# Kernel optimization log

Hardware: AMD Instinct MI355X
Metric: run time of the kernel (lower is better)

The kernel has to match this reference:

```python
import jax, jax.numpy as jnp
import numpy as np

D = 4096       # embed_dim
H = 16         # num_heads
HD = D // H    # head_dim = 256
MLP_H = int(D * 2.0)  # 8192
L_V = 2048
L_T = 1024
GAMMA = 0.6
NOISE_STD = 0.07
TEMP = 0.05
LN_EPS = 1e-5


def setup_inputs() -> dict:
    key = jax.random.key(0)
    ks = jax.random.split(key, 16)
    s = 0.02
    return {
        "vision_feature": jax.random.normal(ks[0], (L_V, D), jnp.float32),
        "text_embed": jax.random.normal(ks[1], (L_T, D), jnp.float32),
        "attention_mask": jnp.zeros((L_T,), jnp.float32),  # additive mask, 0 = attend
        "noise": jax.random.normal(ks[2], (L_V,), jnp.float32),
        "Wq": jax.random.normal(ks[3], (D, D), jnp.float32) * s,
        "bq": jnp.zeros((D,), jnp.float32),
        "Wk": jax.random.normal(ks[4], (D, D), jnp.float32) * s,
        "bk": jnp.zeros((D,), jnp.float32),
        "Wv": jax.random.normal(ks[5], (D, D), jnp.float32) * s,
        "bv": jnp.zeros((D,), jnp.float32),
        "Wo": jax.random.normal(ks[6], (D, D), jnp.float32) * s,
        "bo": jnp.zeros((D,), jnp.float32),
        "ln_w": jnp.ones((D,), jnp.float32),
        "ln_b": jnp.zeros((D,), jnp.float32),
        "W1": jax.random.normal(ks[7], (MLP_H, D), jnp.float32) * s,
        "b1": jnp.zeros((MLP_H,), jnp.float32),
        "W2": jax.random.normal(ks[8], (1, MLP_H), jnp.float32) * s,
        "b2": jnp.zeros((1,), jnp.float32),
    }


def reference(vision_feature, text_embed, attention_mask, noise,
              Wq, bq, Wk, bk, Wv, bv, Wo, bo, ln_w, ln_b, W1, b1, W2, b2):
    # --- cross attention (vision queries over text keys/values) ---
    q = (vision_feature @ Wq.T + bq).reshape(L_V, H, HD)
    k = (text_embed @ Wk.T + bk).reshape(L_T, H, HD)
    v = (text_embed @ Wv.T + bv).reshape(L_T, H, HD)
    logits = jnp.einsum('qhd,khd->hqk', q, k) / np.float32(np.sqrt(HD))
    logits = logits + attention_mask[None, None, :]  # additive attn_mask
    attn = jax.nn.softmax(logits, axis=-1)
    ctx = jnp.einsum('hqk,khd->qhd', attn, v).reshape(L_V, D)
    attn_out = ctx @ Wo.T + bo
    # --- residual + layernorm ---
    x = vision_feature + attn_out
    mu = jnp.mean(x, axis=-1, keepdims=True)
    var = jnp.mean(jnp.square(x - mu), axis=-1, keepdims=True)
    xn = (x - mu) / jnp.sqrt(var + LN_EPS) * ln_w + ln_b
    # --- tiny MLP scorer ---
    h = jax.nn.gelu(xn @ W1.T + b1, approximate=False)
    weight_scores = (h @ W2.T + b2)[:, 0] + noise * NOISE_STD
    # --- temperature softmax over all tokens, top-p (gamma) selection ---
    p = jax.nn.softmax(weight_scores / TEMP, axis=0)
    order = jnp.argsort(-p)           # descending sort indices
    cum = jnp.cumsum(p[order])
    keep = cum <= GAMMA               # threshold_index prefix mask
    gathered = vision_feature[order]  # [L_V, D]
    # fixed-shape stand-in for indices[:threshold_index] gather:
    # valid selected rows are the nonzero prefix
    return jnp.where(keep[:, None], gathered, jnp.zeros((), gathered.dtype))
```

## Files before the change

kernel.cpp:

```cpp
#include <hip/hip_runtime.h>
#include <math.h>


#define LV   2048
#define LT   1024
#define DIM  4096
#define NHD  16
#define HDD  256
#define MLPH 8192

typedef __attribute__((ext_vector_type(8))) short bfx8;
typedef __attribute__((ext_vector_type(4))) float fx4;
typedef unsigned short u16;

__device__ __forceinline__ float wave_sum(float v){
#pragma unroll
  for (int o = 32; o > 0; o >>= 1) v += __shfl_xor(v, o);
  return v;
}
__device__ __forceinline__ float wave_max(float v){
#pragma unroll
  for (int o = 32; o > 0; o >>= 1) v = fmaxf(v, __shfl_xor(v, o));
  return v;
}

__device__ __forceinline__ void splitpack(const float4 a, const float4 b,
                                          bfx8* hi, bfx8* lo){
  float f[8] = {a.x,a.y,a.z,a.w, b.x,b.y,b.z,b.w};
  union { bfx8 v; unsigned u[4]; } H, L;
#pragma unroll
  for (int p = 0; p < 4; ++p){
    unsigned u0 = __float_as_uint(f[2*p]);
    unsigned u1 = __float_as_uint(f[2*p+1]);
    H.u[p] = (u0 >> 16) | (u1 & 0xffff0000u);
    float h0 = __uint_as_float(u0 & 0xffff0000u);
    float h1 = __uint_as_float(u1 & 0xffff0000u);
    unsigned v0 = __float_as_uint(f[2*p]   - h0);
    unsigned v1 = __float_as_uint(f[2*p+1] - h1);
    L.u[p] = (v0 >> 16) | (v1 & 0xffff0000u);
  }
  *hi = H.v; *lo = L.v;
}

__device__ __forceinline__ void glds16(const void* g, void* l){
  __builtin_amdgcn_global_load_lds(
      (const __attribute__((address_space(1))) unsigned int*)g,
      (__attribute__((address_space(3))) unsigned int*)l, 16, 0, 0);
}

__global__ __launch_bounds__(256)
void repack_kernel(const float* __restrict__ src, u16* __restrict__ hi,
                   u16* __restrict__ lo, int Kc, int ktsh)
{
  const long long e = ((long long)blockIdx.x * 256 + threadIdx.x) * 8;
  const int T = (int)(e >> 9);
  const int L = (int)(e >> 3) & 63;
  const int rt = T >> ktsh, kt = T & ((1 << ktsh) - 1);
  const int r = (rt << 4) + (L & 15);
  const int k = (kt << 5) + ((L >> 4) << 3);
  const float* p = src + (long long)r * Kc + k;
  bfx8 h, l;
  splitpack(*(const float4*)p, *(const float4*)(p + 4), &h, &l);
  *(bfx8*)(hi + e) = h;
  *(bfx8*)(lo + e) = l;
}

template<int GELU, int TRANSC>
__global__ __launch_bounds__(256)
void mgemm(const u16* __restrict__ Ah, const u16* __restrict__ Al, int aKT, long long aZe,
           const u16* __restrict__ Bh, const u16* __restrict__ Bl, int bKT, long long bZe,
           float* __restrict__ C, int ldc, long long cZe,
           const float* __restrict__ bias,
           int nx, int KT, int kt0, int zkt, float alpha)
{
  __shared__ bfx8 lbuf[32][64];
  const int tid  = threadIdx.x;
  const int lane = tid & 63;
  const int wv   = tid >> 6;
  const int wr   = wv >> 1, wc = wv & 1;
  const int nwg  = gridDim.x;
  const int id   = blockIdx.x;
  int bm, bn;
  {
    const int my = nwg / nx;
    if (((nx & 3) == 0) && ((my & 1) == 0) && ((nwg & 7) == 0)){
      const int rm = my >> 1, rn = nx >> 2;
      const int x  = id & 7;
      const int j  = id >> 3;
      bm = ((x >> 2) * rm) + j / rn;
      bn = ((x & 3) * rn) + j % rn;
    } else if (((my & 7) == 0) && ((nwg & 7) == 0)){
      const int rm = my >> 3;
      const int x = id & 7, j = id >> 3;
      bm = x * rm + j / nx;
      bn = j % nx;
    } else { bm = id / nx; bn = id % nx; }
  }
  const int m0 = bm << 7;
  const int n0 = bn << 7;
  const int z    = blockIdx.z;
  const u16* Ahz = Ah + (long long)z * aZe;
  const u16* Alz = Al + (long long)z * aZe;
  const u16* Bhz = Bh + (long long)z * bZe;
  const u16* Blz = Bl + (long long)z * bZe;
  C += (long long)z * cZe;
  const int ktb  = kt0 + z * zkt;
  const int rtA0 = m0 >> 4, rtB0 = n0 >> 4;

  const fx4 zz = {0.f, 0.f, 0.f, 0.f};
  fx4 acc[4][4];
#pragma unroll
  for (int i = 0; i < 4; ++i)
#pragma unroll
    for (int j = 0; j < 4; ++j) acc[i][j] = zz;

  const u16* wbase = (wv == 0) ? Ahz : (wv == 1) ? Alz : (wv == 2) ? Bhz : Blz;
  const int  wrt0  = (wv < 2) ? rtA0 : rtB0;
  const int  wKT   = (wv < 2) ? aKT  : bKT;

  for (int t = 0; t < KT; ++t){
#pragma unroll
    for (int q = 0; q < 8; ++q){
      const u16* g = wbase + ((long long)(wrt0 + q) * wKT + (ktb + t)) * 512
                     + lane * 8;
      glds16((const void*)g, (void*)&lbuf[wv * 8 + q][0]);
    }
    __syncthreads();
    bfx8 ah[4], al[4], bh[4], bl[4];
#pragma unroll
    for (int i = 0; i < 4; ++i){
      ah[i] = lbuf[     wr*4 + i][lane];
      al[i] = lbuf[ 8 + wr*4 + i][lane];
      bh[i] = lbuf[16 + wc*4 + i][lane];
      bl[i] = lbuf[24 + wc*4 + i][lane];
    }
#pragma unroll
    for (int i = 0; i < 4; ++i)
#pragma unroll
      for (int j = 0; j < 4; ++j){
        acc[i][j] = __builtin_amdgcn_mfma_f32_16x16x32_bf16(ah[i], bl[j], acc[i][j], 0, 0, 0);
        acc[i][j] = __builtin_amdgcn_mfma_f32_16x16x32_bf16(al[i], bh[j], acc[i][j], 0, 0, 0);
        acc[i][j] = __builtin_amdgcn_mfma_f32_16x16x32_bf16(ah[i], bh[j], acc[i][j], 0, 0, 0);
      }
    __syncthreads();
  }

#pragma unroll
  for (int i = 0; i < 4; ++i){
    const int row0 = m0 + wr*64 + i*16 + ((lane >> 4) << 2);
#pragma unroll
    for (int j = 0; j < 4; ++j){
      const int col = n0 + wc*64 + j*16 + (lane & 15);
      const float bb = bias ? bias[col] : 0.0f;
      if (TRANSC){
        float4 o;
        o.x = alpha*acc[i][j][0] + bb;
        o.y = alpha*acc[i][j][1] + bb;
        o.z = alpha*acc[i][j][2] + bb;
        o.w = alpha*acc[i][j][3] + bb;
        *(float4*)(C + (size_t)col*ldc + row0) = o;
      } else {
#pragma unroll
        for (int r = 0; r < 4; ++r){
          float v = alpha*acc[i][j][r] + bb;
          if (GELU) v = 0.5f*v*(1.0f + erff(v*0.70710678f));
          C[(size_t)(row0 + r)*ldc + col] = v;
        }
      }
    }
  }
}

template<int GELU, int TRANSC>
__global__ __launch_bounds__(256)
void mgemm_fb(const float* __restrict__ A, long long aZ, int lda,
              const float* __restrict__ B, long long bZ, int ldb,
              float* __restrict__ C, long long cZ, int ldc,
              const float* __restrict__ bias, int Kd, float alpha)
{
  __shared__ bfx8 AhS[512], AlS[512], BhS[512], BlS[512];
  const int tid  = threadIdx.x;
  const int lane = tid & 63;
  const int wv   = tid >> 6;
  const int wr   = wv >> 1, wc = wv & 1;
  const int m0 = blockIdx.y * 128, n0 = blockIdx.x * 128;
  A += (long long)blockIdx.z * aZ;
  B += (long long)blockIdx.z * bZ;
  C += (long long)blockIdx.z * cZ;

  const fx4 zz = {0.f, 0.f, 0.f, 0.f};
  fx4 acc[4][4];
#pragma unroll
  for (int i = 0; i < 4; ++i)
#pragma unroll
    for (int j = 0; j < 4; ++j) acc[i][j] = zz;

  for (int k0 = 0; k0 < Kd; k0 += 32){
    __syncthreads();
#pragma unroll
    for (int pass = 0; pass < 2; ++pass){
      const int s = pass*256 + tid;
      const int m = ((s >> 6) << 4) + (s & 15);
      const int j = (s >> 4) & 3;
      const float* pA = A + (size_t)(m0 + m)*lda + k0 + j*8;
      splitpack(*(const float4*)pA, *(const float4*)(pA + 4), &AhS[s], &AlS[s]);
      const float* pB = B + (size_t)(n0 + m)*ldb + k0 + j*8;
      splitpack(*(const float4*)pB, *(const float4*)(pB + 4), &BhS[s], &BlS[s]);
    }
    __syncthreads();
    bfx8 ah[4], al[4], bh[4], bl[4];
#pragma unroll
    for (int i = 0; i < 4; ++i){
      ah[i] = AhS[(wr*4 + i)*64 + lane];
      al[i] = AlS[(wr*4 + i)*64 + lane];
      bh[i] = BhS[(wc*4 + i)*64 + lane];
      bl[i] = BlS[(wc*4 + i)*64 + lane];
    }
#pragma unroll
    for (int i = 0; i < 4; ++i)
#pragma unroll
      for (int j = 0; j < 4; ++j){
        acc[i][j] = __builtin_amdgcn_mfma_f32_16x16x32_bf16(ah[i], bl[j], acc[i][j], 0, 0, 0);
        acc[i][j] = __builtin_amdgcn_mfma_f32_16x16x32_bf16(al[i], bh[j], acc[i][j], 0, 0, 0);
        acc[i][j] = __builtin_amdgcn_mfma_f32_16x16x32_bf16(ah[i], bh[j], acc[i][j], 0, 0, 0);
      }
  }
#pragma unroll
  for (int i = 0; i < 4; ++i){
    const int row0 = m0 + wr*64 + i*16 + ((lane >> 4) << 2);
#pragma unroll
    for (int j = 0; j < 4; ++j){
      const int col = n0 + wc*64 + j*16 + (lane & 15);
      const float bb = bias ? bias[col] : 0.0f;
      if (TRANSC){
        float4 o;
        o.x = alpha*acc[i][j][0] + bb;
        o.y = alpha*acc[i][j][1] + bb;
        o.z = alpha*acc[i][j][2] + bb;
        o.w = alpha*acc[i][j][3] + bb;
        *(float4*)(C + (size_t)col*ldc + row0) = o;
      } else {
#pragma unroll
        for (int r = 0; r < 4; ++r){
          float v = alpha*acc[i][j][r] + bb;
          if (GELU) v = 0.5f*v*(1.0f + erff(v*0.70710678f));
          C[(size_t)(row0 + r)*ldc + col] = v;
        }
      }
    }
  }
}

__global__ __launch_bounds__(128)
void softmax_pack(const float* __restrict__ Lf, u16* __restrict__ ph,
                  u16* __restrict__ pl)
{
  __shared__ float rr[4];
  const int tid = threadIdx.x;
  const int h = blockIdx.x >> 11;
  const int m = blockIdx.x & 2047;
  const float* row = Lf + ((long long)h * 2048 + m) * 1024;
  const int k = tid * 8;
  float4 a = *(const float4*)(row + k);
  float4 b = *(const float4*)(row + k + 4);
  float v[8] = {a.x,a.y,a.z,a.w, b.x,b.y,b.z,b.w};
  float mx = v[0];
#pragma unroll
  for (int i = 1; i < 8; ++i) mx = fmaxf(mx, v[i]);
  mx = wave_max(mx);
  if ((tid & 63) == 0) rr[tid >> 6] = mx;
  __syncthreads();
  const float M = fmaxf(rr[0], rr[1]);
  float e[8], s = 0.0f;
#pragma unroll
  for (int i = 0; i < 8; ++i){ e[i] = expf(v[i] - M); s += e[i]; }
  s = wave_sum(s);
  if ((tid & 63) == 0) rr[2 + (tid >> 6)] = s;
  __syncthreads();
  const float S = rr[2] + rr[3];
  float4 p0 = make_float4(e[0]/S, e[1]/S, e[2]/S, e[3]/S);
  float4 p1 = make_float4(e[4]/S, e[5]/S, e[6]/S, e[7]/S);
  bfx8 hh, ll;
  splitpack(p0, p1, &hh, &ll);
  const int tile = (m >> 4) * 32 + (k >> 5);
  const int Lw = ((k >> 3) & 3) * 16 + (m & 15);
  const long long eoff = (long long)h * (2048ll*1024) + (long long)tile * 512 + Lw * 8;
  *(bfx8*)(ph + eoff) = hh;
  *(bfx8*)(pl + eoff) = ll;
}

__global__ __launch_bounds__(256)
void softmax_fb(float* __restrict__ X)
{
  __shared__ float r[8];
  const int tid = threadIdx.x;
  float* row = X + (size_t)blockIdx.x * 1024;
  float4 v = ((const float4*)row)[tid];
  float m = fmaxf(fmaxf(v.x,v.y), fmaxf(v.z,v.w));
  m = wave_max(m);
  if ((tid & 63) == 0) r[tid >> 6] = m;
  __syncthreads();
  m = fmaxf(fmaxf(r[0],r[1]), fmaxf(r[2],r[3]));
  float e0 = expf(v.x - m), e1 = expf(v.y - m), e2 = expf(v.z - m), e3 = expf(v.w - m);
  float s = (e0 + e1) + (e2 + e3);
  s = wave_sum(s);
  if ((tid & 63) == 0) r[4 + (tid >> 6)] = s;
  __syncthreads();
  s = (r[4] + r[5]) + (r[6] + r[7]);
  ((float4*)row)[tid] = make_float4(e0/s, e1/s, e2/s, e3/s);
}

template<int PACK>
__global__ __launch_bounds__(256)
void ln_kernel(const float* __restrict__ vis, const float* ao, float* xnf,
               u16* __restrict__ xh, u16* __restrict__ xl,
               const float* __restrict__ w, const float* __restrict__ b)
{
  __shared__ float r[8];
  __shared__ float stat[2];
  const int tid = threadIdx.x;
  const int m = blockIdx.x;
  const size_t base = (size_t)m * DIM + tid * 16;
  float x[16];
#pragma unroll
  for (int q = 0; q < 4; ++q){
    float4 a = *(const float4*)(vis + base + q*4);
    float4 c = *(const float4*)(ao  + base + q*4);
    x[q*4+0]=a.x+c.x; x[q*4+1]=a.y+c.y; x[q*4+2]=a.z+c.z; x[q*4+3]=a.w+c.w;
  }
  float s = 0.0f;
#pragma unroll
  for (int i = 0; i < 16; ++i) s += x[i];
  s = wave_sum(s);
  if ((tid & 63) == 0) r[tid >> 6] = s;
  __syncthreads();
  if (tid == 0) stat[0] = (r[0]+r[1]+r[2]+r[3]) * (1.0f/4096.0f);
  __syncthreads();
  const float mu = stat[0];
  float vs = 0.0f;
#pragma unroll
  for (int i = 0; i < 16; ++i){ float d = x[i]-mu; vs += d*d; }
  vs = wave_sum(vs);
  if ((tid & 63) == 0) r[4 + (tid >> 6)] = vs;
  __syncthreads();
  if (tid == 0) stat[1] = (r[4]+r[5]+r[6]+r[7]) * (1.0f/4096.0f);
  __syncthreads();
  const float inv = 1.0f / sqrtf(stat[1] + 1e-5f);
  const int col = tid * 16;
  float o[16];
#pragma unroll
  for (int q = 0; q < 4; ++q){
    float4 wv = *(const float4*)(w + col + q*4);
    float4 bv = *(const float4*)(b + col + q*4);
    o[q*4+0] = (x[q*4+0]-mu)*inv*wv.x + bv.x;
    o[q*4+1] = (x[q*4+1]-mu)*inv*wv.y + bv.y;
    o[q*4+2] = (x[q*4+2]-mu)*inv*wv.z + bv.z;
    o[q*4+3] = (x[q*4+3]-mu)*inv*wv.w + bv.w;
  }
  if (PACK){
#pragma unroll
    for (int q = 0; q < 2; ++q){
      const int k = col + q*8;
      float4 p0 = make_float4(o[q*8+0], o[q*8+1], o[q*8+2], o[q*8+3]);
      float4 p1 = make_float4(o[q*8+4], o[q*8+5], o[q*8+6], o[q*8+7]);
      bfx8 hh, ll;
      splitpack(p0, p1, &hh, &ll);
      const int tile = (m >> 4) * 128 + (k >> 5);
      const int Lw = ((k >> 3) & 3) * 16 + (m & 15);
      const long long e = (long long)tile * 512 + Lw * 8;
      *(bfx8*)(xh + e) = hh;
      *(bfx8*)(xl + e) = ll;
    }
  } else {
#pragma unroll
    for (int q = 0; q < 4; ++q)
      *(float4*)(xnf + base + q*4) = make_float4(o[q*4+0],o[q*4+1],o[q*4+2],o[q*4+3]);
  }
}

__global__ __launch_bounds__(256)
void score_kernel(const float* __restrict__ H1, const float* __restrict__ W2v,
                  const float* __restrict__ b2, const float* __restrict__ noise,
                  float* __restrict__ sc)
{
  __shared__ float r[4];
  const int tid = threadIdx.x;
  const float* h = H1 + (size_t)blockIdx.x * MLPH + tid * 32;
  const float* w = W2v + tid * 32;
  float s = 0.0f;
#pragma unroll
  for (int q = 0; q < 8; ++q){
    float4 a = *(const float4*)(h + q*4);
    float4 c = *(const float4*)(w + q*4);
    s += a.x*c.x + a.y*c.y + a.z*c.z + a.w*c.w;
  }
  s = wave_sum(s);
  if ((tid & 63) == 0) r[tid >> 6] = s;
  __syncthreads();
  if (tid == 0) sc[blockIdx.x] = (r[0]+r[1]+r[2]+r[3]) + b2[0] + noise[blockIdx.x]*0.07f;
}

__global__ __launch_bounds__(1024)
void select_kernel(const float* __restrict__ scores,
                   int* __restrict__ ord, int* __restrict__ kcount)
{
  __shared__ float sv[LV];
  __shared__ int   si[LV];
  __shared__ float red[32];
  __shared__ float stat[2];
  const int tid = threadIdx.x;
  for (int i = tid; i < LV; i += 1024){ sv[i] = scores[i] / 0.05f; si[i] = i; }
  __syncthreads();
  float m = -3.4e38f;
  for (int i = tid; i < LV; i += 1024) m = fmaxf(m, sv[i]);
  m = wave_max(m);
  if ((tid & 63) == 0) red[tid >> 6] = m;
  __syncthreads();
  if (tid == 0){
    float M = red[0];
    for (int w = 1; w < 16; ++w) M = fmaxf(M, red[w]);
    stat[0] = M;
  }
  __syncthreads();
  const float ymax = stat[0];
  float d = 0.0f;
  for (int i = tid; i < LV; i += 1024) d += expf(sv[i] - ymax);
  d = wave_sum(d);
  if ((tid & 63) == 0) red[16 + (tid >> 6)] = d;
  __syncthreads();
  if (tid == 0){
    float D = 0.0f;
    for (int w = 0; w < 16; ++w) D += red[16 + w];
    stat[1] = D;
  }
  __syncthreads();
  const float denom = stat[1];
  for (int size = 2; size <= LV; size <<= 1){
    for (int stride = size >> 1; stride > 0; stride >>= 1){
      __syncthreads();
      const int i = 2*tid - (tid & (stride - 1));
      const int j = i + stride;
      const bool up = ((i & size) == 0);
      float a = sv[i], b = sv[j];
      if ((a < b) == up){
        sv[i] = b; sv[j] = a;
        int ti = si[i]; si[i] = si[j]; si[j] = ti;
      }
    }
  }
  __syncthreads();
  for (int i = tid; i < LV; i += 1024) sv[i] = expf(sv[i] - ymax) / denom;
  __syncthreads();
  if (tid == 0){
    float c = 0.0f; int kc = LV;
    for (int j = 0; j < LV; ++j){
      c += sv[j];
      if (!((double)c <= 0.6)){ kc = j; break; }
    }
    *kcount = kc;
  }
  __syncthreads();
  for (int i = tid; i < LV; i += 1024) ord[i] = si[i];
}

__global__ __launch_bounds__(256)
void writer_kernel(const float* __restrict__ vis, const int* __restrict__ ord,
                   const int* __restrict__ kc, float* __restrict__ out)
{
  const int j = blockIdx.x;
  float4* dst = (float4*)(out + (size_t)j * DIM);
  if (j < kc[0]){
    const float4* src = (const float4*)(vis + (size_t)ord[j] * DIM);
    for (int i = threadIdx.x; i < DIM/4; i += 256) dst[i] = src[i];
  } else {
    const float4 z4 = make_float4(0.f,0.f,0.f,0.f);
    for (int i = threadIdx.x; i < DIM/4; i += 256) dst[i] = z4;
  }
}

extern "C" void kernel_launch(void* const* d_in, const int* in_sizes, int n_in,
                              void* d_out, int out_size, void* d_ws, size_t ws_size,
                              hipStream_t stream)
{
  (void)in_sizes; (void)n_in; (void)out_size;
  const float* vis  = (const float*)d_in[0];
  const float* txt  = (const float*)d_in[1];
  const float* mask = (const float*)d_in[2];
  const float* noise= (const float*)d_in[3];
  const float* Wq = (const float*)d_in[4];  const float* bq = (const float*)d_in[5];
  const float* Wk = (const float*)d_in[6];  const float* bk = (const float*)d_in[7];
  const float* Wv = (const float*)d_in[8];  const float* bv = (const float*)d_in[9];
  const float* Wo = (const float*)d_in[10]; const float* bo = (const float*)d_in[11];
  const float* lw = (const float*)d_in[12]; const float* lb = (const float*)d_in[13];
  const float* W1 = (const float*)d_in[14]; const float* b1 = (const float*)d_in[15];
  const float* W2 = (const float*)d_in[16]; const float* b2 = (const float*)d_in[17];
  float* out = (float*)d_out;
  const dim3 blk(256);
  const size_t MiB = 1u << 20;

  int Hc = 0;
  for (int h = 16; h >= 1; h >>= 1){
    size_t need = (192 + 16 * (size_t)h) * MiB;
    if (need <= ws_size){ Hc = h; break; }
  }

  if (Hc > 0){
    char* B0 = (char*)d_ws;
    u16* WSh  = (u16*)(B0 + 0);          u16* WSl  = (u16*)(B0 + 32*MiB);
    float* TMPf = (float*)(B0 + 64*MiB);
    u16* QCh  = (u16*)(B0 + 96*MiB);     u16* QCl  = (u16*)(B0 + 112*MiB);
    u16* VCh  = (u16*)(B0 + 128*MiB);    u16* VCl  = (u16*)(B0 + 144*MiB);
    u16* TCh  = (u16*)(B0 + 160*MiB);    u16* TCl  = (u16*)(B0 + 168*MiB);
    float* KF  = (float*)(B0 + 176*MiB);
    float* VTF = (float*)(B0 + 192*MiB);
    u16* VTCh = (u16*)(B0 + 176*MiB);    u16* VTCl = (u16*)(B0 + 184*MiB);
    float* Lf  = (float*)(B0 + 192*MiB);
    u16* PCh  = (u16*)(B0 + (192 + (size_t)Hc*8)*MiB);
    u16* PCl  = (u16*)(B0 + (192 + (size_t)Hc*12)*MiB);
    float* H1f = (float*)(B0 + 128*MiB);
    u16* XNh  = (u16*)(B0 + 96*MiB);     u16* XNl  = (u16*)(B0 + 112*MiB);
    float* SCf = (float*)(B0 + 192*MiB);
    int* ORD = (int*)(SCf + LV);
    int* KCp = ORD + LV;

    repack_kernel<<<dim3(4096), blk, 0, stream>>>(vis, VCh, VCl, 4096, 7);
    repack_kernel<<<dim3(2048), blk, 0, stream>>>(txt, TCh, TCl, 4096, 7);
    repack_kernel<<<dim3(8192), blk, 0, stream>>>(Wq, WSh, WSl, 4096, 7);
    mgemm<0,0><<<dim3(512,1,1), blk, 0, stream>>>(VCh, VCl, 128, 0, WSh, WSl, 128, 0,
        TMPf, 4096, 0, bq, 32, 128, 0, 0, 1.0f);
    repack_kernel<<<dim3(8192), blk, 0, stream>>>(Wk, WSh, WSl, 4096, 7);
    mgemm<0,0><<<dim3(256,1,1), blk, 0, stream>>>(TCh, TCl, 128, 0, WSh, WSl, 128, 0,
        KF, 4096, 0, bk, 32, 128, 0, 0, 1.0f);
    repack_kernel<<<dim3(8192), blk, 0, stream>>>(Wv, WSh, WSl, 4096, 7);
    mgemm<0,1><<<dim3(256,1,1), blk, 0, stream>>>(TCh, TCl, 128, 0, WSh, WSl, 128, 0,
        VTF, 1024, 0, bv, 32, 128, 0, 0, 1.0f);
    repack_kernel<<<dim3(4096), blk, 0, stream>>>(TMPf, QCh, QCl, 4096, 7);
    repack_kernel<<<dim3(2048), blk, 0, stream>>>(KF, TCh, TCl, 4096, 7);
    repack_kernel<<<dim3(2048), blk, 0, stream>>>(VTF, VTCh, VTCl, 1024, 5);
    const int NG = NHD / Hc;
    for (int g = 0; g < NG; ++g){
      mgemm<0,0><<<dim3(128,1,Hc), blk, 0, stream>>>(QCh, QCl, 128, 0, TCh, TCl, 128, 0,
          Lf, 1024, 2097152ll, mask, 8, 8, g*Hc*8, 8, 0.0625f);
      softmax_pack<<<dim3(Hc*2048), dim3(128), 0, stream>>>(Lf, PCh, PCl);
      mgemm<0,0><<<dim3(32,1,Hc), blk, 0, stream>>>(PCh, PCl, 32, 2097152ll,
          VTCh + (long long)g*Hc*262144, VTCl + (long long)g*Hc*262144, 32, 262144ll,
          TMPf + (long long)g*Hc*256, 4096, 256, nullptr, 2, 32, 0, 0, 1.0f);
    }
    repack_kernel<<<dim3(4096), blk, 0, stream>>>(TMPf, VCh, VCl, 4096, 7);
    repack_kernel<<<dim3(8192), blk, 0, stream>>>(Wo, WSh, WSl, 4096, 7);
    mgemm<0,0><<<dim3(512,1,1), blk, 0, stream>>>(VCh, VCl, 128, 0, WSh, WSl, 128, 0,
        TMPf, 4096, 0, bo, 32, 128, 0, 0, 1.0f);
    ln_kernel<1><<<dim3(LV), blk, 0, stream>>>(vis, TMPf, nullptr, XNh, XNl, lw, lb);
    repack_kernel<<<dim3(8192), blk, 0, stream>>>(W1, WSh, WSl, 4096, 7);
    mgemm<1,0><<<dim3(512,1,1), blk, 0, stream>>>(XNh, XNl, 128, 0, WSh, WSl, 128, 0,
        H1f, 8192, 0, b1, 32, 128, 0, 0, 1.0f);
    repack_kernel<<<dim3(8192), blk, 0, stream>>>(W1 + 16777216ll, WSh, WSl, 4096, 7);
    mgemm<1,0><<<dim3(512,1,1), blk, 0, stream>>>(XNh, XNl, 128, 0, WSh, WSl, 128, 0,
        H1f + 4096, 8192, 0, b1 + 4096, 32, 128, 0, 0, 1.0f);
    score_kernel<<<dim3(LV), blk, 0, stream>>>(H1f, W2, b2, noise, SCf);
    select_kernel<<<dim3(1), dim3(1024), 0, stream>>>(SCf, ORD, KCp);
    writer_kernel<<<dim3(LV), blk, 0, stream>>>(vis, ORD, KCp, out);
    return;
  }

  float* ws = (float*)d_ws;
  const long long OQ  = 0;
  const long long OK_ = (long long)LV * DIM;
  const long long OV  = OK_ + (long long)LT * DIM;
  const long long OC  = OV  + (long long)LT * DIM;
  const long long OL  = OC  + (long long)LV * DIM;
  const long long LSTRIDE = (long long)LV * LT;
  int Hf = 16;
  while (Hf > 1){
    size_t need = (size_t)(OL + (long long)Hf * LSTRIDE + 8192) * 4;
    if (need <= ws_size) break;
    Hf >>= 1;
  }
  float* Qw  = ws + OQ;
  float* Kw  = ws + OK_;
  float* Vt  = ws + OV;
  float* Cw  = ws + OC;
  float* Lw  = ws + OL;
  float* H1w = ws + OK_;
  float* SCw = ws + OL + (long long)Hf * LSTRIDE;
  int*   ORDw = (int*)(SCw + LV);
  int*   KCw  = ORDw + LV;

  mgemm_fb<0,0><<<dim3(DIM/128, LV/128, 1), blk, 0, stream>>>(vis,0,DIM, Wq,0,DIM, Qw,0,DIM, bq, DIM, 1.0f);
  mgemm_fb<0,0><<<dim3(DIM/128, LT/128, 1), blk, 0, stream>>>(txt,0,DIM, Wk,0,DIM, Kw,0,DIM, bk, DIM, 1.0f);
  mgemm_fb<0,1><<<dim3(DIM/128, LT/128, 1), blk, 0, stream>>>(txt,0,DIM, Wv,0,DIM, Vt,0,LT, bv, DIM, 1.0f);
  for (int g = 0; g < NHD/Hf; ++g){
    const long long ho = (long long)g * Hf * HDD;
    mgemm_fb<0,0><<<dim3(LT/128, LV/128, Hf), blk, 0, stream>>>(
        Qw+ho, HDD, DIM,  Kw+ho, HDD, DIM,  Lw, LSTRIDE, LT,  mask, HDD, 0.0625f);
    softmax_fb<<<dim3(Hf*LV), blk, 0, stream>>>(Lw);
    mgemm_fb<0,0><<<dim3(HDD/128, LV/128, Hf), blk, 0, stream>>>(
        Lw, LSTRIDE, LT,  Vt + (ho*(long long)LT), (long long)HDD*LT, LT,
        Cw+ho, HDD, DIM,  nullptr, LT, 1.0f);
  }
  mgemm_fb<0,0><<<dim3(DIM/128, LV/128, 1), blk, 0, stream>>>(Cw,0,DIM, Wo,0,DIM, Qw,0,DIM, bo, DIM, 1.0f);
  ln_kernel<0><<<dim3(LV), blk, 0, stream>>>(vis, Qw, Qw, nullptr, nullptr, lw, lb);
  mgemm_fb<1,0><<<dim3(MLPH/128, LV/128, 1), blk, 0, stream>>>(Qw,0,DIM, W1,0,DIM, H1w,0,MLPH, b1, DIM, 1.0f);
  score_kernel<<<dim3(LV), blk, 0, stream>>>(H1w, W2, b2, noise, SCw);
  select_kernel<<<dim3(1), dim3(1024), 0, stream>>>(SCw, ORDw, KCw);
  writer_kernel<<<dim3(LV), blk, 0, stream>>>(vis, ORDw, KCw, out);
}
```

Before: 1.643 ms.

## Fuse weight split-packing into GEMM loads and double-buffer LDS tiles

Adds a GEMM variant that reads fp32 weight rows directly, splits them into bf16 hi/lo in registers and writes them to shared memory. This removes the six separate weight repack kernels and their workspace round-trips. Both GEMM kernels now double-buffer the LDS tiles, so the next k-tile is fetched while MFMAs run on the current one. The cost is doubled LDS use, which may lower occupancy, and redundant per-block conversion of the weight tile across row blocks.

```diff
diff --git a/kernel.cpp b/kernel.cpp
--- a/kernel.cpp
+++ b/kernel.cpp
@@ -46,6 +46,23 @@
   __builtin_amdgcn_global_load_lds(
       (const __attribute__((address_space(1))) unsigned int*)g,
       (__attribute__((address_space(3))) unsigned int*)l, 16, 0, 0);
+}
+
+__device__ __forceinline__ void xcd_swizzle(int id, int nwg, int nx,
+                                            int* bm, int* bn){
+  const int my = nwg / nx;
+  if (((nx & 3) == 0) && ((my & 1) == 0) && ((nwg & 7) == 0)){
+    const int rm = my >> 1, rn = nx >> 2;
+    const int x  = id & 7;
+    const int j  = id >> 3;
+    *bm = ((x >> 2) * rm) + j / rn;
+    *bn = ((x & 3) * rn) + j % rn;
+  } else if (((my & 7) == 0) && ((nwg & 7) == 0)){
+    const int rm = my >> 3;
+    const int x = id & 7, j = id >> 3;
+    *bm = x * rm + j / nx;
+    *bn = j % nx;
+  } else { *bm = id / nx; *bn = id % nx; }
 }
 
 __global__ __launch_bounds__(256)
@@ -73,29 +90,13 @@
            const float* __restrict__ bias,
            int nx, int KT, int kt0, int zkt, float alpha)
 {
-  __shared__ bfx8 lbuf[32][64];
+  __shared__ bfx8 lbuf[2][32][64];
   const int tid  = threadIdx.x;
   const int lane = tid & 63;
   const int wv   = tid >> 6;
   const int wr   = wv >> 1, wc = wv & 1;
-  const int nwg  = gridDim.x;
-  const int id   = blockIdx.x;
   int bm, bn;
-  {
-    const int my = nwg / nx;
-    if (((nx & 3) == 0) && ((my & 1) == 0) && ((nwg & 7) == 0)){
-      const int rm = my >> 1, rn = nx >> 2;
-      const int x  = id & 7;
-      const int j  = id >> 3;
-      bm = ((x >> 2) * rm) + j / rn;
-      bn = ((x & 3) * rn) + j % rn;
-    } else if (((my & 7) == 0) && ((nwg & 7) == 0)){
-      const int rm = my >> 3;
-      const int x = id & 7, j = id >> 3;
-      bm = x * rm + j / nx;
-      bn = j % nx;
-    } else { bm = id / nx; bn = id % nx; }
-  }
+  xcd_swizzle(blockIdx.x, gridDim.x, nx, &bm, &bn);
   const int m0 = bm << 7;
   const int n0 = bn << 7;
   const int z    = blockIdx.z;
@@ -118,21 +119,28 @@
   const int  wrt0  = (wv < 2) ? rtA0 : rtB0;
   const int  wKT   = (wv < 2) ? aKT  : bKT;
 
+#define STAGE(BUF, KTI)                                                        \
+  {                                                                            \
+    _Pragma("unroll")                                                          \
+    for (int q = 0; q < 8; ++q){                                               \
+      const u16* g = wbase + ((long long)(wrt0 + q) * wKT + (KTI)) * 512       \
+                     + lane * 8;                                               \
+      glds16((const void*)g, (void*)&lbuf[BUF][wv * 8 + q][0]);                \
+    }                                                                          \
+  }
+
+  int cur = 0;
+  STAGE(0, ktb);
   for (int t = 0; t < KT; ++t){
-#pragma unroll
-    for (int q = 0; q < 8; ++q){
-      const u16* g = wbase + ((long long)(wrt0 + q) * wKT + (ktb + t)) * 512
-                     + lane * 8;
-      glds16((const void*)g, (void*)&lbuf[wv * 8 + q][0]);
-    }
     __syncthreads();
+    if (t + 1 < KT) STAGE(cur ^ 1, ktb + t + 1);
     bfx8 ah[4], al[4], bh[4], bl[4];
 #pragma unroll
     for (int i = 0; i < 4; ++i){
-      ah[i] = lbuf[     wr*4 + i][lane];
-      al[i] = lbuf[ 8 + wr*4 + i][lane];
-      bh[i] = lbuf[16 + wc*4 + i][lane];
-      bl[i] = lbuf[24 + wc*4 + i][lane];
+      ah[i] = lbuf[cur][     wr*4 + i][lane];
+      al[i] = lbuf[cur][ 8 + wr*4 + i][lane];
+      bh[i] = lbuf[cur][16 + wc*4 + i][lane];
+      bl[i] = lbuf[cur][24 + wc*4 + i][lane];
     }
 #pragma unroll
     for (int i = 0; i < 4; ++i)
@@ -142,8 +150,136 @@
         acc[i][j] = __builtin_amdgcn_mfma_f32_16x16x32_bf16(al[i], bh[j], acc[i][j], 0, 0, 0);
         acc[i][j] = __builtin_amdgcn_mfma_f32_16x16x32_bf16(ah[i], bh[j], acc[i][j], 0, 0, 0);
       }
+    cur ^= 1;
+  }
+#undef STAGE
+
+#pragma unroll
+  for (int i = 0; i < 4; ++i){
+    const int row0 = m0 + wr*64 + i*16 + ((lane >> 4) << 2);
+#pragma unroll
+    for (int j = 0; j < 4; ++j){
+      const int col = n0 + wc*64 + j*16 + (lane & 15);
+      const float bb = bias ? bias[col] : 0.0f;
+      if (TRANSC){
+        float4 o;
+        o.x = alpha*acc[i][j][0] + bb;
+        o.y = alpha*acc[i][j][1] + bb;
+        o.z = alpha*acc[i][j][2] + bb;
+        o.w = alpha*acc[i][j][3] + bb;
+        *(float4*)(C + (size_t)col*ldc + row0) = o;
+      } else {
+#pragma unroll
+        for (int r = 0; r < 4; ++r){
+          float v = alpha*acc[i][j][r] + bb;
+          if (GELU) v = 0.5f*v*(1.0f + erff(v*0.70710678f));
+          C[(size_t)(row0 + r)*ldc + col] = v;
+        }
+      }
+    }
+  }
+}
+
+template<int GELU, int TRANSC>
+__global__ __launch_bounds__(256)
+void mgemm_wb(const u16* __restrict__ Ah, const u16* __restrict__ Al, int aKT,
+              const float* __restrict__ Bf, int ldb,
+              float* __restrict__ C, int ldc,
+              const float* __restrict__ bias,
+              int nx, int KT, float alpha)
+{
+  __shared__ bfx8 lbuf[2][32][64];
+  const int tid  = threadIdx.x;
+  const int lane = tid & 63;
+  const int wv   = tid >> 6;
+  const int wr   = wv >> 1, wc = wv & 1;
+  int bm, bn;
+  xcd_swizzle(blockIdx.x, gridDim.x, nx, &bm, &bn);
+  const int m0 = bm << 7;
+  const int n0 = bn << 7;
+  const int rtA0 = m0 >> 4;
+
+  const fx4 zz = {0.f, 0.f, 0.f, 0.f};
+  fx4 acc[4][4];
+#pragma unroll
+  for (int i = 0; i < 4; ++i)
+#pragma unroll
+    for (int j = 0; j < 4; ++j) acc[i][j] = zz;
+
+#define STAGE_A(BUF, KTI)                                                      \
+  {                                                                            \
+    _Pragma("unroll")                                                          \
+    for (int q = 0; q < 4; ++q){                                               \
+      const int u = wv*4 + q;                                                  \
+      const u16* base = (u < 8) ? Ah : Al;                                     \
+      const u16* g = base + ((long long)(rtA0 + (u & 7)) * aKT + (KTI)) * 512  \
+                     + lane * 8;                                               \
+      glds16((const void*)g, (void*)&lbuf[BUF][u][0]);                         \
+    }                                                                          \
+  }
+
+  const int brow = tid >> 1;
+  const int bo   = (tid & 1) << 4;
+  const int bu   = 16 + (brow >> 4);
+  const int bL0  = ((bo >> 3) << 4) + (brow & 15);
+  const int bL1  = bL0 + 16;
+  const float* bp = Bf + (size_t)(n0 + brow) * ldb + bo;
+
+#define STAGE_B(BUF, B0, B1, B2, B3)                                           \
+  {                                                                            \
+    bfx8 h0, l0, h1, l1;                                                       \
+    splitpack(B0, B1, &h0, &l0);                                               \
+    splitpack(B2, B3, &h1, &l1);                                               \
+    lbuf[BUF][bu    ][bL0] = h0;                                               \
+    lbuf[BUF][bu    ][bL1] = h1;                                               \
+    lbuf[BUF][bu + 8][bL0] = l0;                                               \
+    lbuf[BUF][bu + 8][bL1] = l1;                                               \
+  }
+
+  {
+    const float* p = bp;
+    float4 b0 = *(const float4*)(p + 0);
+    float4 b1 = *(const float4*)(p + 4);
+    float4 b2 = *(const float4*)(p + 8);
+    float4 b3 = *(const float4*)(p + 12);
+    STAGE_B(0, b0, b1, b2, b3);
+    STAGE_A(0, 0);
+  }
+
+  int cur = 0;
+  for (int t = 0; t < KT; ++t){
     __syncthreads();
-  }
+    float4 b0, b1, b2, b3;
+    const bool pre = (t + 1 < KT);
+    if (pre){
+      const float* p = bp + (size_t)(t + 1) * 32;
+      b0 = *(const float4*)(p + 0);
+      b1 = *(const float4*)(p + 4);
+      b2 = *(const float4*)(p + 8);
+      b3 = *(const float4*)(p + 12);
+      STAGE_A(cur ^ 1, t + 1);
+    }
+    bfx8 ah[4], al[4], bh[4], bl[4];
+#pragma unroll
+    for (int i = 0; i < 4; ++i){
+      ah[i] = lbuf[cur][     wr*4 + i][lane];
+      al[i] = lbuf[cur][ 8 + wr*4 + i][lane];
+      bh[i] = lbuf[cur][16 + wc*4 + i][lane];
+      bl[i] = lbuf[cur][24 + wc*4 + i][lane];
+    }
+#pragma unroll
+    for (int i = 0; i < 4; ++i)
+#pragma unroll
+      for (int j = 0; j < 4; ++j){
+        acc[i][j] = __builtin_amdgcn_mfma_f32_16x16x32_bf16(ah[i], bl[j], acc[i][j], 0, 0, 0);
+        acc[i][j] = __builtin_amdgcn_mfma_f32_16x16x32_bf16(al[i], bh[j], acc[i][j], 0, 0, 0);
+        acc[i][j] = __builtin_amdgcn_mfma_f32_16x16x32_bf16(ah[i], bh[j], acc[i][j], 0, 0, 0);
+      }
+    if (pre) STAGE_B(cur ^ 1, b0, b1, b2, b3);
+    cur ^= 1;
+  }
+#undef STAGE_A
+#undef STAGE_B
 
 #pragma unroll
   for (int i = 0; i < 4; ++i){
@@ -506,7 +642,6 @@
 
   if (Hc > 0){
     char* B0 = (char*)d_ws;
-    u16* WSh  = (u16*)(B0 + 0);          u16* WSl  = (u16*)(B0 + 32*MiB);
     float* TMPf = (float*)(B0 + 64*MiB);
     u16* QCh  = (u16*)(B0 + 96*MiB);     u16* QCl  = (u16*)(B0 + 112*MiB);
     u16* VCh  = (u16*)(B0 + 128*MiB);    u16* VCl  = (u16*)(B0 + 144*MiB);
@@ -525,15 +660,12 @@
 
     repack_kernel<<<dim3(4096), blk, 0, stream>>>(vis, VCh, VCl, 4096, 7);
     repack_kernel<<<dim3(2048), blk, 0, stream>>>(txt, TCh, TCl, 4096, 7);
-    repack_kernel<<<dim3(8192), blk, 0, stream>>>(Wq, WSh, WSl, 4096, 7);
-    mgemm<0,0><<<dim3(512,1,1), blk, 0, stream>>>(VCh, VCl, 128, 0, WSh, WSl, 128, 0,
-        TMPf, 4096, 0, bq, 32, 128, 0, 0, 1.0f);
-    repack_kernel<<<dim3(8192), blk, 0, stream>>>(Wk, WSh, WSl, 4096, 7);
-    mgemm<0,0><<<dim3(256,1,1), blk, 0, stream>>>(TCh, TCl, 128, 0, WSh, WSl, 128, 0,
-        KF, 4096, 0, bk, 32, 128, 0, 0, 1.0f);
-    repack_kernel<<<dim3(8192), blk, 0, stream>>>(Wv, WSh, WSl, 4096, 7);
-    mgemm<0,1><<<dim3(256,1,1), blk, 0, stream>>>(TCh, TCl, 128, 0, WSh, WSl, 128, 0,
-        VTF, 1024, 0, bv, 32, 128, 0, 0, 1.0f);
+    mgemm_wb<0,0><<<dim3(512,1,1), blk, 0, stream>>>(VCh, VCl, 128, Wq, 4096,
+        TMPf, 4096, bq, 32, 128, 1.0f);
+    mgemm_wb<0,0><<<dim3(256,1,1), blk, 0, stream>>>(TCh, TCl, 128, Wk, 4096,
+        KF, 4096, bk, 32, 128, 1.0f);
+    mgemm_wb<0,1><<<dim3(256,1,1), blk, 0, stream>>>(TCh, TCl, 128, Wv, 4096,
+        VTF, 1024, bv, 32, 128, 1.0f);
     repack_kernel<<<dim3(4096), blk, 0, stream>>>(TMPf, QCh, QCl, 4096, 7);
     repack_kernel<<<dim3(2048), blk, 0, stream>>>(KF, TCh, TCl, 4096, 7);
     repack_kernel<<<dim3(2048), blk, 0, stream>>>(VTF, VTCh, VTCl, 1024, 5);
@@ -547,16 +679,13 @@
           TMPf + (long long)g*Hc*256, 4096, 256, nullptr, 2, 32, 0, 0, 1.0f);
     }
     repack_kernel<<<dim3(4096), blk, 0, stream>>>(TMPf, VCh, VCl, 4096, 7);
-    repack_kernel<<<dim3(8192), blk, 0, stream>>>(Wo, WSh, WSl, 4096, 7);
-    mgemm<0,0><<<dim3(512,1,1), blk, 0, stream>>>(VCh, VCl, 128, 0, WSh, WSl, 128, 0,
-        TMPf, 4096, 0, bo, 32, 128, 0, 0, 1.0f);
+    mgemm_wb<0,0><<<dim3(512,1,1), blk, 0, stream>>>(VCh, VCl, 128, Wo, 4096,
+        TMPf, 4096, bo, 32, 128, 1.0f);
     ln_kernel<1><<<dim3(LV), blk, 0, stream>>>(vis, TMPf, nullptr, XNh, XNl, lw, lb);
-    repack_kernel<<<dim3(8192), blk, 0, stream>>>(W1, WSh, WSl, 4096, 7);
-    mgemm<1,0><<<dim3(512,1,1), blk, 0, stream>>>(XNh, XNl, 128, 0, WSh, WSl, 128, 0,
-        H1f, 8192, 0, b1, 32, 128, 0, 0, 1.0f);
-    repack_kernel<<<dim3(8192), blk, 0, stream>>>(W1 + 16777216ll, WSh, WSl, 4096, 7);
-    mgemm<1,0><<<dim3(512,1,1), blk, 0, stream>>>(XNh, XNl, 128, 0, WSh, WSl, 128, 0,
-        H1f + 4096, 8192, 0, b1 + 4096, 32, 128, 0, 0, 1.0f);
+    mgemm_wb<1,0><<<dim3(512,1,1), blk, 0, stream>>>(XNh, XNl, 128, W1, 4096,
+        H1f, 8192, b1, 32, 128, 1.0f);
+    mgemm_wb<1,0><<<dim3(512,1,1), blk, 0, stream>>>(XNh, XNl, 128, W1 + 16777216ll, 4096,
+        H1f + 4096, 8192, b1 + 4096, 32, 128, 1.0f);
     score_kernel<<<dim3(LV), blk, 0, stream>>>(H1f, W2, b2, noise, SCf);
     select_kernel<<<dim3(1), dim3(1024), 0, stream>>>(SCf, ORD, KCp);
     writer_kernel<<<dim3(LV), blk, 0, stream>>>(vis, ORD, KCp, out);
```

Measured after the change: 1.889 ms. 15.0% more time.
